# Kernel optimization log

Hardware: AMD Instinct MI355X
Metric: run time of the kernel (lower is better)

The kernel has to match this reference:

```python
import jax, jax.numpy as jnp
import numpy as np

D_MODEL = 1024
D_INNER = 1024
N_HEADS = 16
D_HEAD = D_INNER // N_HEADS
B = 2
CUR = 1024
PREV = 1024
LN_EPS = 1e-5


def _rel_shift(x):
    # x: (b, i, j, h) -- faithful to torch: pad along i, flat-reinterpret, drop first row
    b, i, j, h = x.shape
    zp = jnp.zeros((b, 1, j, h), x.dtype)
    xp = jnp.concatenate([zp, x], axis=1).reshape(i + 1, b, j, h)
    return xp[1:].reshape(b, i, j, h)


def setup_inputs() -> dict:
    key = jax.random.key(0)
    ks = jax.random.split(key, 10)
    x = jax.random.normal(ks[0], (B, CUR, D_MODEL), jnp.float32)
    mem = jax.random.normal(ks[1], (B, PREV, D_MODEL), jnp.float32)
    pos_emb = jax.random.normal(ks[2], (CUR + PREV, D_INNER), jnp.float32)
    u = jax.random.normal(ks[3], (N_HEADS, D_HEAD), jnp.float32) * 0.02
    v = jax.random.normal(ks[4], (N_HEADS, D_HEAD), jnp.float32) * 0.02
    # causal mask: query i (current segment) may attend key j if j <= i + PREV
    idx_i = jnp.arange(CUR)[:, None]
    idx_j = jnp.arange(CUR + PREV)[None, :]
    tgt_mask = jnp.broadcast_to((idx_j > idx_i + PREV)[None, :, :, None], (B, CUR, CUR + PREV, 1))
    Wq = jax.random.normal(ks[5], (D_INNER, D_MODEL), jnp.float32) * 0.02
    Wkv = jax.random.normal(ks[6], (2 * D_INNER, D_MODEL), jnp.float32) * 0.02
    Wfc = jax.random.normal(ks[7], (D_MODEL, D_INNER), jnp.float32) * 0.02
    bfc = jnp.zeros((D_MODEL,), jnp.float32)
    gamma = jnp.ones((D_MODEL,), jnp.float32)
    beta = jnp.zeros((D_MODEL,), jnp.float32)
    return {"x": x, "pos_emb": pos_emb, "u": u, "v": v, "mem": mem,
            "tgt_mask": tgt_mask, "Wq": Wq, "Wkv": Wkv, "Wfc": Wfc,
            "bfc": bfc, "gamma": gamma, "beta": beta}


def reference(x, pos_emb, u, v, mem, tgt_mask, Wq, Wkv, Wfc, bfc, gamma, beta):
    b, cur, _ = x.shape
    prev = mem.shape[1]
    tot = cur + prev
    h_telda = jnp.concatenate([mem, x], axis=1)               # (b, tot, d_model)
    q = jnp.einsum('bsm,im->bsi', x, Wq)                      # (b, cur, d_inner)
    kv = jnp.einsum('bsm,im->bsi', h_telda, Wkv)              # (b, tot, 2*d_inner)
    k, vv = kv[..., :D_INNER], kv[..., D_INNER:]
    q = q.reshape(b, cur, N_HEADS, D_HEAD)
    k = k.reshape(b, tot, N_HEADS, D_HEAD)
    vv = vv.reshape(b, tot, N_HEADS, D_HEAD)
    content = jnp.einsum('bihd,bjhd->bijh', q + u, k)
    pos = pos_emb.reshape(tot, N_HEADS, D_HEAD)
    pos_attn = jnp.einsum('bihd,jhd->bijh', q + v, pos)
    attn = content + _rel_shift(pos_attn)
    attn = jnp.where(tgt_mask, -jnp.inf, attn)
    attn = attn / (D_HEAD ** 0.5)
    attn = jax.nn.softmax(attn, axis=1)  # faithful: softmax over query dim as in original
    out = jnp.einsum('bijh,bjhd->bihd', attn, vv).reshape(b, cur, D_INNER)
    y = x + jnp.einsum('bsi,mi->bsm', out, Wfc) + bfc
    mu = jnp.mean(y, axis=-1, keepdims=True)
    var = jnp.mean((y - mu) ** 2, axis=-1, keepdims=True)
    return (y - mu) / jnp.sqrt(var + LN_EPS) * gamma + beta
```

## Files before the change

### kernel.cpp

```cpp
#include <hip/hip_runtime.h>
#include <hip/hip_bf16.h>
#include <stdint.h>

typedef unsigned short u16;
typedef __attribute__((ext_vector_type(8))) __bf16 bf16x8;
typedef __attribute__((ext_vector_type(4))) float f32x4;
typedef __attribute__((ext_vector_type(4))) float float4v;
typedef __attribute__((ext_vector_type(4))) u16  u16x4;

#define DEV __device__ __forceinline__

#define NB   2
#define CUR  1024
#define PREV 1024
#define TOT  2048
#define DM   1024
#define NH   16
#define DH   64

DEV u16 f2b(float f) {
    uint32_t u = __builtin_bit_cast(uint32_t, f);
    uint32_t r = (u + 0x7fffu + ((u >> 16) & 1u)) >> 16;
    return (u16)r;
}
DEV float b2f(u16 u) {
    return __builtin_bit_cast(float, (uint32_t)u << 16);
}

typedef const __attribute__((address_space(1))) void* gptr_t;
typedef __attribute__((address_space(3))) void*       lptr_t;
DEV void async16(const void* g, void* l) {
    __builtin_amdgcn_global_load_lds((gptr_t)g, (lptr_t)l, 16, 0, 0);
}

template<int BM, int BN, int BK, int WM, int WN, int EPI>
__global__ __launch_bounds__(256)
void gemm_bt(const u16* __restrict__ A, const u16* __restrict__ B,
             int M, int N, int K, long sA, long sB, int bzBase,
             void* __restrict__ C0, void* __restrict__ C1,
             const float* __restrict__ F0, const float* __restrict__ F1)
{
    constexpr int WAVES_N = BN / WN;
    constexpr int MI = WM / 16, NI = WN / 16;
    static_assert((BM / WM) * (BN / WN) == 4, "4 waves");
    static_assert(BK == 64, "swizzle assumes 8 chunks/row");

    __shared__ u16 lA[BM * BK];
    __shared__ u16 lB[BN * BK];

    const int bz = blockIdx.z;
    const int m0 = blockIdx.y * BM, n0 = blockIdx.x * BN;
    const int tid = threadIdx.x, wave = tid >> 6, lane = tid & 63;

    const u16* Ab = A + (long)bz * sA;
    const u16* Bb = B + (long)bz * sB;
    const int wm0 = (wave / WAVES_N) * WM, wn0 = (wave % WAVES_N) * WN;
    const int quad = lane >> 4;

    f32x4 acc[MI][NI];
#pragma unroll
    for (int mi = 0; mi < MI; ++mi)
#pragma unroll
        for (int ni = 0; ni < NI; ++ni)
            acc[mi][ni] = f32x4{0.f, 0.f, 0.f, 0.f};

    const int srow = tid >> 3;
    const int ksw  = (((tid & 7) ^ ((tid >> 3) & 7)) << 3);

    for (int kt = 0; kt < K; kt += BK) {
        __syncthreads();
#pragma unroll
        for (int is = 0; is < (BM * BK) / 2048; ++is) {
            int r = is * 32 + srow;
            async16(Ab + (long)(m0 + r) * K + kt + ksw, &lA[is * 2048 + wave * 512]);
        }
#pragma unroll
        for (int is = 0; is < (BN * BK) / 2048; ++is) {
            int r = is * 32 + srow;
            async16(Bb + (long)(n0 + r) * K + kt + ksw, &lB[is * 2048 + wave * 512]);
        }
        __syncthreads();
#pragma unroll
        for (int ks = 0; ks < BK; ks += 32) {
            bf16x8 af[MI], br[NI];
#pragma unroll
            for (int mi = 0; mi < MI; ++mi)
                af[mi] = *(const bf16x8*)(const void*)
                    &lA[(wm0 + mi * 16 + (lane & 15)) * BK +
                        ((((ks >> 3) + quad) ^ (lane & 7)) << 3)];
#pragma unroll
            for (int ni = 0; ni < NI; ++ni)
                br[ni] = *(const bf16x8*)(const void*)
                    &lB[(wn0 + ni * 16 + (lane & 15)) * BK +
                        ((((ks >> 3) + quad) ^ (lane & 7)) << 3)];
#pragma unroll
            for (int mi = 0; mi < MI; ++mi)
#pragma unroll
                for (int ni = 0; ni < NI; ++ni)
                    acc[mi][ni] = __builtin_amdgcn_mfma_f32_16x16x32_bf16(af[mi], br[ni], acc[mi][ni], 0, 0, 0);
        }
    }

    const int gbz = bzBase + bz;

    if constexpr (EPI == 1) {
        u16* Abuf = (u16*)C0;
        const int b = gbz;
#pragma unroll
        for (int mi = 0; mi < MI; ++mi) {
            const int m = m0 + wm0 + mi * 16 + quad * 4;
            const int h = m >> 6, d = m & 63;
            const float4v uu = *(const float4v*)(F0 + m);
            const float4v vv = *(const float4v*)(F1 + m);
#pragma unroll
            for (int ni = 0; ni < NI; ++ni) {
                const int i = n0 + wn0 + ni * 16 + (lane & 15);
                u16x4 pu, pv;
#pragma unroll
                for (int r = 0; r < 4; ++r) {
                    pu[r] = f2b(acc[mi][ni][r] + uu[r]);
                    pv[r] = f2b(acc[mi][ni][r] + vv[r]);
                }
                *(u16x4*)(Abuf + (((long)(b * NH + h)) * CUR + i) * 128 + d) = pu;
                if (b == 0) {
                    if (i > 0)
                        *(u16x4*)(Abuf + (((long)h) * CUR + (i - 1)) * 128 + 64 + d) = pv;
                    if (i == 1023) {
                        u16x4 z = {};
                        *(u16x4*)(Abuf + (((long)h) * CUR + 1023) * 128 + 64 + d) = z;
                    }
                } else {
                    *(u16x4*)(Abuf + (((long)(NH + h)) * CUR + i) * 128 + 64 + d) = pv;
                }
            }
        }
    } else if constexpr (EPI == 2) {
#pragma unroll
        for (int mi = 0; mi < MI; ++mi) {
            const int m = m0 + wm0 + mi * 16 + quad * 4;
            const bool isV = m >= DM;
            const int h = (m >> 6) & 15, d = m & 63;
#pragma unroll
            for (int ni = 0; ni < NI; ++ni) {
                const int n = n0 + wn0 + ni * 16 + (lane & 15);
                const int b = n >> 11, j = n & 2047;
                u16x4 p;
#pragma unroll
                for (int r = 0; r < 4; ++r) p[r] = f2b(acc[mi][ni][r]);
                if (!isV)
                    *(u16x4*)((u16*)C0 + (((long)(b * NH + h)) * TOT + j) * 128 + d) = p;
                else
                    *(u16x4*)((u16*)C1 + (((long)(b * NH + h)) * TOT + j) * 64 + d) = p;
            }
        }
    } else if constexpr (EPI == 5) {
#pragma unroll
        for (int mi = 0; mi < MI; ++mi) {
            const int m = m0 + wm0 + mi * 16 + quad * 4;
            const float4v bb = *(const float4v*)(F1 + m);
#pragma unroll
            for (int ni = 0; ni < NI; ++ni) {
                const int n = n0 + wn0 + ni * 16 + (lane & 15);
                const float4v xr = *(const float4v*)(F0 + (long)n * DM + m);
                float4v y;
#pragma unroll
                for (int r = 0; r < 4; ++r) y[r] = xr[r] + acc[mi][ni][r] + bb[r];
                *(float4v*)((float*)C0 + (long)n * DM + m) = y;
            }
        }
    }
}

template<int DO_PV>
__global__ __launch_bounds__(256)
void fused_attn(const u16* __restrict__ Abuf, const u16* __restrict__ Bbuf,
                const u16* __restrict__ Vp, const float* __restrict__ rcs,
                float* __restrict__ colsum, u16* __restrict__ Opart)
{
    __shared__ u16 lQ[64 * 128];
    __shared__ u16 lK[64 * 128];
    __shared__ u16 lV[DO_PV ? 64 * 64 : 1];
    __shared__ u16 lP[DO_PV ? 64 * 64 : 1];

    const int it = 15 - (int)blockIdx.x;
    const int bh = blockIdx.y;
    const int ch = blockIdx.z;
    const int n0 = it * 64;
    const int b = bh >> 4, h = bh & 15;
    const int tid = threadIdx.x, wave = tid >> 6, lane = tid & 63;
    const int l15 = lane & 15, quad = lane >> 4;
    const int iw = wave * 16 + l15;

    const u16*  Qg = Abuf + ((long)bh * CUR + n0) * 128;
    const u16*  Kg = Bbuf + (long)bh * TOT * 128;
    const u16*  Vg = Vp + (long)bh * DH * TOT;
    const float* rc = rcs + (long)bh * TOT;
    float* CS = colsum + (long)bh * TOT;

    const int r4 = tid >> 4, c4 = tid & 15;
    const int csQ = ((c4 & 8) | ((c4 & 7) ^ (r4 & 7)));
    const int r8 = tid >> 3;
    const int csV = (tid & 7) ^ (r8 & 7);

#pragma unroll
    for (int is = 0; is < 4; ++is)
        async16(Qg + (long)(is * 16 + r4) * 128 + csQ * 8, &lQ[is * 2048 + wave * 512]);

    f32x4 oacc[4];
#pragma unroll
    for (int mi = 0; mi < 4; ++mi) oacc[mi] = f32x4{0.f, 0.f, 0.f, 0.f};

    const int ig = n0 + iw;
    const int nt = it + 17;
    const int half = (nt + 1) >> 1;
    const int t0 = ch ? half : 0;
    const int t1 = ch ? nt : half;

    for (int t = t0; t < t1; ++t) {
        const int j0 = t * 64;
        __syncthreads();
        {
#pragma unroll
            for (int is = 0; is < 4; ++is)
                async16(Kg + (long)(j0 + is * 16 + r4) * 128 + csQ * 8,
                        &lK[is * 2048 + wave * 512]);
        }
        if constexpr (DO_PV) {
#pragma unroll
            for (int is = 0; is < 2; ++is)
                async16(Vg + (long)(is * 32 + r8) * TOT + j0 + csV * 8,
                        &lV[is * 2048 + wave * 512]);
        }
        __syncthreads();

        if constexpr (DO_PV) {
            f32x4 sacc[4];
#pragma unroll
            for (int smi = 0; smi < 4; ++smi) sacc[smi] = f32x4{0.f, 0.f, 0.f, 0.f};
#pragma unroll
            for (int ks = 0; ks < 128; ks += 32) {
                const int cq = (ks >> 3) + quad;
                const bf16x8 qf = *(const bf16x8*)(const void*)
                    &lQ[iw * 128 + (((cq & 8) | ((cq & 7) ^ (iw & 7))) << 3)];
#pragma unroll
                for (int smi = 0; smi < 4; ++smi) {
                    const int jr = smi * 16 + l15;
                    const bf16x8 kf = *(const bf16x8*)(const void*)
                        &lK[jr * 128 + (((cq & 8) | ((cq & 7) ^ (jr & 7))) << 3)];
                    sacc[smi] = __builtin_amdgcn_mfma_f32_16x16x32_bf16(kf, qf, sacc[smi], 0, 0, 0);
                }
            }
#pragma unroll
            for (int smi = 0; smi < 4; ++smi) {
                const int jl = smi * 16 + quad * 4;
                const int jg = j0 + jl;
                const float4v rcv = *(const float4v*)(rc + jg);
                u16x4 pk;
#pragma unroll
                for (int r = 0; r < 4; ++r) {
                    float p = (jg + r > ig + PREV) ? 0.f : __expf(sacc[smi][r] * 0.125f) * rcv[r];
                    pk[r] = f2b(p);
                }
                const int c16 = (jl >> 3) ^ (iw & 7);
                *(u16x4*)&lP[iw * 64 + (c16 << 3) + ((quad & 1) << 2)] = pk;
            }
#pragma unroll
            for (int ks = 0; ks < 64; ks += 32) {
                const int cp = (ks >> 3) + quad;
                const bf16x8 pb = *(const bf16x8*)(const void*)
                    &lP[iw * 64 + ((cp ^ (iw & 7)) << 3)];
#pragma unroll
                for (int mi = 0; mi < 4; ++mi) {
                    const int dr = mi * 16 + l15;
                    const bf16x8 vf = *(const bf16x8*)(const void*)
                        &lV[dr * 64 + ((cp ^ (dr & 7)) << 3)];
                    oacc[mi] = __builtin_amdgcn_mfma_f32_16x16x32_bf16(vf, pb, oacc[mi], 0, 0, 0);
                }
            }
        } else {
            f32x4 sacc[4];
#pragma unroll
            for (int smi = 0; smi < 4; ++smi) sacc[smi] = f32x4{0.f, 0.f, 0.f, 0.f};
#pragma unroll
            for (int ks = 0; ks < 128; ks += 32) {
                const int cq = (ks >> 3) + quad;
                const bf16x8 kf = *(const bf16x8*)(const void*)
                    &lK[iw * 128 + (((cq & 8) | ((cq & 7) ^ (iw & 7))) << 3)];
#pragma unroll
                for (int smi = 0; smi < 4; ++smi) {
                    const int ir = smi * 16 + l15;
                    const bf16x8 qf = *(const bf16x8*)(const void*)
                        &lQ[ir * 128 + (((cq & 8) | ((cq & 7) ^ (ir & 7))) << 3)];
                    sacc[smi] = __builtin_amdgcn_mfma_f32_16x16x32_bf16(qf, kf, sacc[smi], 0, 0, 0);
                }
            }
            const int jg = j0 + iw;
            float sum = 0.f;
#pragma unroll
            for (int smi = 0; smi < 4; ++smi) {
#pragma unroll
                for (int r = 0; r < 4; ++r) {
                    const int ii = n0 + smi * 16 + quad * 4 + r;
                    if (jg <= ii + PREV) sum += __expf(sacc[smi][r] * 0.125f);
                }
            }
            sum += __shfl_xor(sum, 16);
            sum += __shfl_xor(sum, 32);
            if (quad == 0) atomicAdd(CS + jg, sum);
        }
    }

    if constexpr (DO_PV) {
        u16* Ob = Opart + ((long)(ch * NB + b) * CUR) * DM + h * DH;
#pragma unroll
        for (int mi = 0; mi < 4; ++mi) {
            const int d = mi * 16 + quad * 4;
            u16x4 p;
#pragma unroll
            for (int r = 0; r < 4; ++r) p[r] = f2b(oacc[mi][r]);
            *(u16x4*)(Ob + (long)ig * DM + d) = p;
        }
    }
}

__global__ __launch_bounds__(256)
void combine_O(const u16* __restrict__ O0, const u16* __restrict__ O1,
               u16* __restrict__ Obf)
{
    int i = blockIdx.x * 256 + threadIdx.x;
    u16x4 a = ((const u16x4*)O0)[i];
    u16x4 c = ((const u16x4*)O1)[i];
    u16x4 o;
#pragma unroll
    for (int r = 0; r < 4; ++r) o[r] = f2b(b2f(a[r]) + b2f(c[r]));
    ((u16x4*)Obf)[i] = o;
}

__global__ __launch_bounds__(256)
void cvt_weights(const float* __restrict__ Wq, const float* __restrict__ Wkv,
                 const float* __restrict__ Wfc, u16* __restrict__ Wqb,
                 u16* __restrict__ Wkvb, u16* __restrict__ Wfcb)
{
    int i = blockIdx.x * 256 + threadIdx.x;
    const float* s; u16* d; int off;
    if (i < 262144)      { s = Wq;  d = Wqb;  off = i; }
    else if (i < 786432) { s = Wkv; d = Wkvb; off = i - 262144; }
    else                 { s = Wfc; d = Wfcb; off = i - 786432; }
    float4v f = ((const float4v*)s)[off];
    u16x4 o = {f2b(f[0]), f2b(f[1]), f2b(f[2]), f2b(f[3])};
    ((u16x4*)d)[off] = o;
}

__global__ __launch_bounds__(256)
void pack_H(const float* __restrict__ mem, const float* __restrict__ x, u16* __restrict__ dst)
{
    int i = blockIdx.x * 256 + threadIdx.x;
    int e = i << 2;
    int b = e >> 21, r = e & ((1 << 21) - 1);
    const float* src = (r < (1 << 20)) ? (mem + ((long)b << 20) + r)
                                       : (x + ((long)b << 20) + (r - (1 << 20)));
    float4v f = *(const float4v*)src;
    u16x4 o = {f2b(f[0]), f2b(f[1]), f2b(f[2]), f2b(f[3])};
    ((u16x4*)dst)[i] = o;
}

__global__ __launch_bounds__(256)
void pack_pos(const float* __restrict__ pos, u16* __restrict__ Bbuf)
{
    int i = blockIdx.x * 256 + threadIdx.x;
    int e = i << 2;
    int h = e >> 17, r = e & 131071, j = r >> 6, d = r & 63;
    float4v f = *(const float4v*)(pos + (long)j * DM + h * DH + d);
    u16x4 o = {f2b(f[0]), f2b(f[1]), f2b(f[2]), f2b(f[3])};
    long base = ((long)h * TOT + j) * 128 + 64 + d;
    *(u16x4*)(Bbuf + base) = o;
    *(u16x4*)(Bbuf + base + (long)NH * TOT * 128) = o;
}

__global__ __launch_bounds__(256)
void vprime_kernel(const u16* __restrict__ Vtmp, const float* __restrict__ colsum,
                   u16* __restrict__ Vp, float* __restrict__ rcs)
{
    __shared__ float t[64][65];
    int bz = blockIdx.y;
    int j0 = blockIdx.x * 64;
    const u16* src = Vtmp + ((long)bz * TOT + j0) * 64;
    const float* cs = colsum + (long)bz * TOT + j0;
    for (int e = threadIdx.x; e < 4096; e += 256) {
        int jl = e >> 6, d = e & 63;
        t[jl][d] = b2f(src[e]);
    }
    if (threadIdx.x < 64)
        rcs[(long)bz * TOT + j0 + threadIdx.x] = 1.f / cs[threadIdx.x];
    __syncthreads();
    u16* dst = Vp + (long)bz * DH * TOT + j0;
    for (int e = threadIdx.x; e < 4096; e += 256) {
        int d = e >> 6, jl = e & 63;
        dst[(long)d * TOT + jl] = f2b(t[jl][d]);
    }
}

__global__ __launch_bounds__(256)
void ln_kernel(const float* __restrict__ Y, const float* __restrict__ gamma,
               const float* __restrict__ beta, float* __restrict__ out)
{
    const int row = blockIdx.x;
    const float* y = Y + (long)row * DM;
    float v[4];
    float s = 0.f;
#pragma unroll
    for (int t = 0; t < 4; ++t) { v[t] = y[threadIdx.x + t * 256]; s += v[t]; }
#pragma unroll
    for (int off = 32; off > 0; off >>= 1) s += __shfl_down(s, off);
    __shared__ float r1[4], r2[4];
    int wv = threadIdx.x >> 6, ln = threadIdx.x & 63;
    if (ln == 0) r1[wv] = s;
    __syncthreads();
    float mu = (r1[0] + r1[1] + r1[2] + r1[3]) * (1.f / DM);
    float q = 0.f;
#pragma unroll
    for (int t = 0; t < 4; ++t) { float d = v[t] - mu; q += d * d; }
#pragma unroll
    for (int off = 32; off > 0; off >>= 1) q += __shfl_down(q, off);
    if (ln == 0) r2[wv] = q;
    __syncthreads();
    float var = (r2[0] + r2[1] + r2[2] + r2[3]) * (1.f / DM);
    float inv = rsqrtf(var + 1e-5f);
#pragma unroll
    for (int t = 0; t < 4; ++t) {
        int c = threadIdx.x + t * 256;
        out[(long)row * DM + c] = (v[t] - mu) * inv * gamma[c] + beta[c];
    }
}

extern "C" void kernel_launch(void* const* d_in, const int* in_sizes, int n_in,
                              void* d_out, int out_size, void* d_ws, size_t ws_size,
                              hipStream_t stream)
{
    const float* x     = (const float*)d_in[0];
    const float* pos   = (const float*)d_in[1];
    const float* u     = (const float*)d_in[2];
    const float* vbias = (const float*)d_in[3];
    const float* mem   = (const float*)d_in[4];
    const float* Wq    = (const float*)d_in[6];
    const float* Wkv   = (const float*)d_in[7];
    const float* Wfc   = (const float*)d_in[8];
    const float* bfc   = (const float*)d_in[9];
    const float* gamma = (const float*)d_in[10];
    const float* beta  = (const float*)d_in[11];
    float* out = (float*)d_out;

    char* w = (char*)d_ws;
    auto alloc = [&](size_t bytes) {
        char* p = w;
        w += (bytes + 255) & ~(size_t)255;
        return p;
    };
    u16*   Hb     = (u16*)alloc(4096UL * 1024 * 2);
    u16*   Wqb    = (u16*)alloc(1024UL * 1024 * 2);
    u16*   Wkvb   = (u16*)alloc(2048UL * 1024 * 2);
    u16*   Wfcb   = (u16*)alloc(1024UL * 1024 * 2);
    u16*   Abuf   = (u16*)alloc(32UL * 1024 * 128 * 2);
    u16*   Bbuf   = (u16*)alloc(32UL * 2048 * 128 * 2);
    u16*   Vtmp   = (u16*)alloc(32UL * 2048 * 64 * 2);
    u16*   Vp     = (u16*)alloc(32UL * 64 * 2048 * 2);
    float* colsum = (float*)alloc(32UL * 2048 * 4);
    float* rcs    = (float*)alloc(32UL * 2048 * 4);
    u16*   Opart  = (u16*)alloc(2UL * 2048 * 1024 * 2);
    u16*   Obf    = (u16*)alloc(2048UL * 1024 * 2);
    float* Yf     = (float*)alloc(2048UL * 1024 * 4);

    hipMemsetAsync(colsum, 0, 32UL * 2048 * 4, stream);

    cvt_weights<<<4096, 256, 0, stream>>>(Wq, Wkv, Wfc, Wqb, Wkvb, Wfcb);
    pack_H  <<<4096, 256, 0, stream>>>(mem, x, Hb);
    pack_pos<<<2048, 256, 0, stream>>>(pos, Bbuf);

    gemm_bt<128, 64, 64, 64, 32, 1><<<dim3(16, 8, 2), 256, 0, stream>>>(
        Wqb, Hb + 1024UL * 1024, 1024, 1024, 1024, 0, 2048L * 1024, 0,
        Abuf, nullptr, u, vbias);
    gemm_bt<128, 128, 64, 64, 64, 2><<<dim3(32, 16, 1), 256, 0, stream>>>(
        Wkvb, Hb, 2048, 4096, 1024, 0, 0, 0, Bbuf, Vtmp, nullptr, nullptr);

    fused_attn<0><<<dim3(16, 32, 2), 256, 0, stream>>>(
        Abuf, Bbuf, nullptr, nullptr, colsum, nullptr);
    vprime_kernel<<<dim3(32, 32), 256, 0, stream>>>(Vtmp, colsum, Vp, rcs);
    fused_attn<1><<<dim3(16, 32, 2), 256, 0, stream>>>(
        Abuf, Bbuf, Vp, rcs, nullptr, Opart);
    combine_O<<<2048, 256, 0, stream>>>(Opart, Opart + 2048UL * 1024, Obf);

    gemm_bt<64, 128, 64, 32, 64, 5><<<dim3(16, 16, 1), 256, 0, stream>>>(
        Wfcb, Obf, 1024, 2048, 1024, 0, 0, 0, Yf, nullptr, x, bfc);
    ln_kernel<<<2048, 256, 0, stream>>>(Yf, gamma, beta, out);
}
```

Baseline: 219.0 us.

## Restructure attention passes to keep K, P and V in registers

The two attention passes now split each 64-key tile across waves (16 keys per wave) instead of splitting query rows. K and V fragments are loaded straight from global memory into registers, and the softmax probabilities stay in registers as MFMA operands, so the per-tile LDS staging and block barriers go away. Each wave accumulates partial O for all 64 query rows, and the partials are summed across waves through LDS at the end. The reciprocal column-sum is now folded into V in vprime, which removes the rcs buffer. In exchange, the PV MFMAs run with half of their K-slots zero-padded, more global loads are uncoalesced, and the kernel holds a larger accumulator register footprint.

```diff
diff --git a/kernel.cpp b/kernel.cpp
--- a/kernel.cpp
+++ b/kernel.cpp
@@ -7,6 +7,7 @@
 typedef __attribute__((ext_vector_type(4))) float f32x4;
 typedef __attribute__((ext_vector_type(4))) float float4v;
 typedef __attribute__((ext_vector_type(4))) u16  u16x4;
+typedef __attribute__((ext_vector_type(8))) u16  u16x8;
 
 #define DEV __device__ __forceinline__
 
@@ -172,153 +173,153 @@
 }
 
 template<int DO_PV>
-__global__ __launch_bounds__(256)
-void fused_attn(const u16* __restrict__ Abuf, const u16* __restrict__ Bbuf,
-                const u16* __restrict__ Vp, const float* __restrict__ rcs,
-                float* __restrict__ colsum, u16* __restrict__ Opart)
+__global__ __launch_bounds__(256, 2)
+void attn2(const u16* __restrict__ Abuf, const u16* __restrict__ Bbuf,
+           const u16* __restrict__ Vp, float* __restrict__ colsum,
+           u16* __restrict__ Opart)
 {
     __shared__ u16 lQ[64 * 128];
-    __shared__ u16 lK[64 * 128];
-    __shared__ u16 lV[DO_PV ? 64 * 64 : 1];
-    __shared__ u16 lP[DO_PV ? 64 * 64 : 1];
+    __shared__ float lO[DO_PV ? 64 * 68 : 1];
 
     const int it = 15 - (int)blockIdx.x;
     const int bh = blockIdx.y;
     const int ch = blockIdx.z;
     const int n0 = it * 64;
-    const int b = bh >> 4, h = bh & 15;
     const int tid = threadIdx.x, wave = tid >> 6, lane = tid & 63;
     const int l15 = lane & 15, quad = lane >> 4;
-    const int iw = wave * 16 + l15;
-
-    const u16*  Qg = Abuf + ((long)bh * CUR + n0) * 128;
-    const u16*  Kg = Bbuf + (long)bh * TOT * 128;
-    const u16*  Vg = Vp + (long)bh * DH * TOT;
-    const float* rc = rcs + (long)bh * TOT;
+
+    const u16* Qg = Abuf + ((long)bh * CUR + n0) * 128;
+    const u16* Kg = Bbuf + (long)bh * TOT * 128;
+    const u16* Vg = Vp + (long)bh * DH * TOT;
     float* CS = colsum + (long)bh * TOT;
 
-    const int r4 = tid >> 4, c4 = tid & 15;
-    const int csQ = ((c4 & 8) | ((c4 & 7) ^ (r4 & 7)));
-    const int r8 = tid >> 3;
-    const int csV = (tid & 7) ^ (r8 & 7);
-
-#pragma unroll
-    for (int is = 0; is < 4; ++is)
-        async16(Qg + (long)(is * 16 + r4) * 128 + csQ * 8, &lQ[is * 2048 + wave * 512]);
-
-    f32x4 oacc[4];
-#pragma unroll
-    for (int mi = 0; mi < 4; ++mi) oacc[mi] = f32x4{0.f, 0.f, 0.f, 0.f};
-
-    const int ig = n0 + iw;
+    {
+        const int r4 = tid >> 4, c4 = tid & 15;
+        const int csQ = (c4 & 8) | ((c4 & 7) ^ (r4 & 7));
+#pragma unroll
+        for (int is = 0; is < 4; ++is)
+            async16(Qg + (long)(is * 16 + r4) * 128 + csQ * 8, &lQ[is * 2048 + wave * 512]);
+    }
+    __syncthreads();
+
+    f32x4 oacc[4][4];
+    if constexpr (DO_PV) {
+#pragma unroll
+        for (int mi = 0; mi < 4; ++mi)
+#pragma unroll
+            for (int smi = 0; smi < 4; ++smi)
+                oacc[mi][smi] = f32x4{0.f, 0.f, 0.f, 0.f};
+    }
+
+    const int jw = wave * 16;
     const int nt = it + 17;
     const int half = (nt + 1) >> 1;
     const int t0 = ch ? half : 0;
     const int t1 = ch ? nt : half;
 
     for (int t = t0; t < t1; ++t) {
-        const int j0 = t * 64;
-        __syncthreads();
-        {
-#pragma unroll
-            for (int is = 0; is < 4; ++is)
-                async16(Kg + (long)(j0 + is * 16 + r4) * 128 + csQ * 8,
-                        &lK[is * 2048 + wave * 512]);
-        }
+        const int jbase = t * 64 + jw;
+        const u16* Krow = Kg + (long)(jbase + l15) * 128 + quad * 8;
+        bf16x8 kreg[4];
+#pragma unroll
+        for (int c = 0; c < 4; ++c)
+            kreg[c] = *(const bf16x8*)(const void*)(Krow + c * 32);
+
+        f32x4 sacc[4];
+#pragma unroll
+        for (int smi = 0; smi < 4; ++smi) sacc[smi] = f32x4{0.f, 0.f, 0.f, 0.f};
+#pragma unroll
+        for (int c = 0; c < 4; ++c) {
+            const int cq = c * 4 + quad;
+#pragma unroll
+            for (int smi = 0; smi < 4; ++smi) {
+                const bf16x8 qf = *(const bf16x8*)(const void*)
+                    &lQ[(smi * 16 + l15) * 128 + (((cq & 8) | ((cq & 7) ^ (l15 & 7))) << 3)];
+                sacc[smi] = __builtin_amdgcn_mfma_f32_16x16x32_bf16(kreg[c], qf, sacc[smi], 0, 0, 0);
+            }
+        }
+
         if constexpr (DO_PV) {
-#pragma unroll
-            for (int is = 0; is < 2; ++is)
-                async16(Vg + (long)(is * 32 + r8) * TOT + j0 + csV * 8,
-                        &lV[is * 2048 + wave * 512]);
-        }
-        __syncthreads();
-
-        if constexpr (DO_PV) {
-            f32x4 sacc[4];
-#pragma unroll
-            for (int smi = 0; smi < 4; ++smi) sacc[smi] = f32x4{0.f, 0.f, 0.f, 0.f};
-#pragma unroll
-            for (int ks = 0; ks < 128; ks += 32) {
-                const int cq = (ks >> 3) + quad;
-                const bf16x8 qf = *(const bf16x8*)(const void*)
-                    &lQ[iw * 128 + (((cq & 8) | ((cq & 7) ^ (iw & 7))) << 3)];
-#pragma unroll
-                for (int smi = 0; smi < 4; ++smi) {
-                    const int jr = smi * 16 + l15;
-                    const bf16x8 kf = *(const bf16x8*)(const void*)
-                        &lK[jr * 128 + (((cq & 8) | ((cq & 7) ^ (jr & 7))) << 3)];
-                    sacc[smi] = __builtin_amdgcn_mfma_f32_16x16x32_bf16(kf, qf, sacc[smi], 0, 0, 0);
-                }
+            bf16x8 vf[4];
+#pragma unroll
+            for (int mi = 0; mi < 4; ++mi) {
+                const u16x4 vl = *(const u16x4*)(Vg + (long)(mi * 16 + l15) * TOT + jbase + quad * 4);
+                const u16x8 vraw = {vl[0], vl[1], vl[2], vl[3], 0, 0, 0, 0};
+                vf[mi] = __builtin_bit_cast(bf16x8, vraw);
             }
 #pragma unroll
             for (int smi = 0; smi < 4; ++smi) {
-                const int jl = smi * 16 + quad * 4;
-                const int jg = j0 + jl;
-                const float4v rcv = *(const float4v*)(rc + jg);
-                u16x4 pk;
-#pragma unroll
-                for (int r = 0; r < 4; ++r) {
-                    float p = (jg + r > ig + PREV) ? 0.f : __expf(sacc[smi][r] * 0.125f) * rcv[r];
-                    pk[r] = f2b(p);
-                }
-                const int c16 = (jl >> 3) ^ (iw & 7);
-                *(u16x4*)&lP[iw * 64 + (c16 << 3) + ((quad & 1) << 2)] = pk;
-            }
-#pragma unroll
-            for (int ks = 0; ks < 64; ks += 32) {
-                const int cp = (ks >> 3) + quad;
-                const bf16x8 pb = *(const bf16x8*)(const void*)
-                    &lP[iw * 64 + ((cp ^ (iw & 7)) << 3)];
-#pragma unroll
-                for (int mi = 0; mi < 4; ++mi) {
-                    const int dr = mi * 16 + l15;
-                    const bf16x8 vf = *(const bf16x8*)(const void*)
-                        &lV[dr * 64 + ((cp ^ (dr & 7)) << 3)];
-                    oacc[mi] = __builtin_amdgcn_mfma_f32_16x16x32_bf16(vf, pb, oacc[mi], 0, 0, 0);
-                }
+                const int ii = n0 + smi * 16 + l15;
+                u16 p0 = 0, p1 = 0, p2 = 0, p3 = 0;
+                const int jq = jbase + quad * 4;
+                if (jq + 0 <= ii + PREV) p0 = f2b(__expf(sacc[smi][0] * 0.125f));
+                if (jq + 1 <= ii + PREV) p1 = f2b(__expf(sacc[smi][1] * 0.125f));
+                if (jq + 2 <= ii + PREV) p2 = f2b(__expf(sacc[smi][2] * 0.125f));
+                if (jq + 3 <= ii + PREV) p3 = f2b(__expf(sacc[smi][3] * 0.125f));
+                const u16x8 praw = {p0, p1, p2, p3, 0, 0, 0, 0};
+                const bf16x8 pb = __builtin_bit_cast(bf16x8, praw);
+#pragma unroll
+                for (int mi = 0; mi < 4; ++mi)
+                    oacc[mi][smi] = __builtin_amdgcn_mfma_f32_16x16x32_bf16(vf[mi], pb, oacc[mi][smi], 0, 0, 0);
             }
         } else {
-            f32x4 sacc[4];
-#pragma unroll
-            for (int smi = 0; smi < 4; ++smi) sacc[smi] = f32x4{0.f, 0.f, 0.f, 0.f};
-#pragma unroll
-            for (int ks = 0; ks < 128; ks += 32) {
-                const int cq = (ks >> 3) + quad;
-                const bf16x8 kf = *(const bf16x8*)(const void*)
-                    &lK[iw * 128 + (((cq & 8) | ((cq & 7) ^ (iw & 7))) << 3)];
-#pragma unroll
-                for (int smi = 0; smi < 4; ++smi) {
-                    const int ir = smi * 16 + l15;
-                    const bf16x8 qf = *(const bf16x8*)(const void*)
-                        &lQ[ir * 128 + (((cq & 8) | ((cq & 7) ^ (ir & 7))) << 3)];
-                    sacc[smi] = __builtin_amdgcn_mfma_f32_16x16x32_bf16(qf, kf, sacc[smi], 0, 0, 0);
-                }
-            }
-            const int jg = j0 + iw;
-            float sum = 0.f;
+            float cs[4] = {0.f, 0.f, 0.f, 0.f};
+            const int jq = jbase + quad * 4;
 #pragma unroll
             for (int smi = 0; smi < 4; ++smi) {
-#pragma unroll
-                for (int r = 0; r < 4; ++r) {
-                    const int ii = n0 + smi * 16 + quad * 4 + r;
-                    if (jg <= ii + PREV) sum += __expf(sacc[smi][r] * 0.125f);
-                }
-            }
-            sum += __shfl_xor(sum, 16);
-            sum += __shfl_xor(sum, 32);
-            if (quad == 0) atomicAdd(CS + jg, sum);
+                const int ii = n0 + smi * 16 + l15;
+#pragma unroll
+                for (int r = 0; r < 4; ++r)
+                    if (jq + r <= ii + PREV) cs[r] += __expf(sacc[smi][r] * 0.125f);
+            }
+#pragma unroll
+            for (int r = 0; r < 4; ++r) {
+                cs[r] += __shfl_xor(cs[r], 1);
+                cs[r] += __shfl_xor(cs[r], 2);
+                cs[r] += __shfl_xor(cs[r], 4);
+                cs[r] += __shfl_xor(cs[r], 8);
+            }
+            if (l15 == 0) {
+                atomicAdd(CS + jq + 0, cs[0]);
+                atomicAdd(CS + jq + 1, cs[1]);
+                atomicAdd(CS + jq + 2, cs[2]);
+                atomicAdd(CS + jq + 3, cs[3]);
+            }
         }
     }
 
     if constexpr (DO_PV) {
+#pragma unroll
+        for (int wv = 0; wv < 4; ++wv) {
+            if (wave == wv) {
+#pragma unroll
+                for (int mi = 0; mi < 4; ++mi)
+#pragma unroll
+                    for (int smi = 0; smi < 4; ++smi) {
+                        const int i = smi * 16 + l15, d = mi * 16 + quad * 4;
+                        float* p = &lO[i * 68 + d];
+                        if (wv == 0) *(f32x4*)p = oacc[mi][smi];
+                        else {
+                            f32x4 cur = *(const f32x4*)p;
+#pragma unroll
+                            for (int r = 0; r < 4; ++r) cur[r] += oacc[mi][smi][r];
+                            *(f32x4*)p = cur;
+                        }
+                    }
+            }
+            __syncthreads();
+        }
+        const int b = bh >> 4, h = bh & 15;
         u16* Ob = Opart + ((long)(ch * NB + b) * CUR) * DM + h * DH;
 #pragma unroll
-        for (int mi = 0; mi < 4; ++mi) {
-            const int d = mi * 16 + quad * 4;
-            u16x4 p;
-#pragma unroll
-            for (int r = 0; r < 4; ++r) p[r] = f2b(oacc[mi][r]);
-            *(u16x4*)(Ob + (long)ig * DM + d) = p;
+        for (int k2 = 0; k2 < 4; ++k2) {
+            const int idx = k2 * 1024 + tid * 4;
+            const int il = idx >> 6, d = idx & 63;
+            const f32x4 vv = *(const f32x4*)&lO[il * 68 + d];
+            u16x4 o;
+#pragma unroll
+            for (int r = 0; r < 4; ++r) o[r] = f2b(vv[r]);
+            *(u16x4*)(Ob + (long)(n0 + il) * DM + d) = o;
         }
     }
 }
@@ -379,7 +380,7 @@
 
 __global__ __launch_bounds__(256)
 void vprime_kernel(const u16* __restrict__ Vtmp, const float* __restrict__ colsum,
-                   u16* __restrict__ Vp, float* __restrict__ rcs)
+                   u16* __restrict__ Vp)
 {
     __shared__ float t[64][65];
     int bz = blockIdx.y;
@@ -388,10 +389,8 @@
     const float* cs = colsum + (long)bz * TOT + j0;
     for (int e = threadIdx.x; e < 4096; e += 256) {
         int jl = e >> 6, d = e & 63;
-        t[jl][d] = b2f(src[e]);
-    }
-    if (threadIdx.x < 64)
-        rcs[(long)bz * TOT + j0 + threadIdx.x] = 1.f / cs[threadIdx.x];
+        t[jl][d] = b2f(src[e]) / cs[jl];
+    }
     __syncthreads();
     u16* dst = Vp + (long)bz * DH * TOT + j0;
     for (int e = threadIdx.x; e < 4096; e += 256) {
@@ -465,7 +464,6 @@
     u16*   Vtmp   = (u16*)alloc(32UL * 2048 * 64 * 2);
     u16*   Vp     = (u16*)alloc(32UL * 64 * 2048 * 2);
     float* colsum = (float*)alloc(32UL * 2048 * 4);
-    float* rcs    = (float*)alloc(32UL * 2048 * 4);
     u16*   Opart  = (u16*)alloc(2UL * 2048 * 1024 * 2);
     u16*   Obf    = (u16*)alloc(2048UL * 1024 * 2);
     float* Yf     = (float*)alloc(2048UL * 1024 * 4);
@@ -482,11 +480,11 @@
     gemm_bt<128, 128, 64, 64, 64, 2><<<dim3(32, 16, 1), 256, 0, stream>>>(
         Wkvb, Hb, 2048, 4096, 1024, 0, 0, 0, Bbuf, Vtmp, nullptr, nullptr);
 
-    fused_attn<0><<<dim3(16, 32, 2), 256, 0, stream>>>(
-        Abuf, Bbuf, nullptr, nullptr, colsum, nullptr);
-    vprime_kernel<<<dim3(32, 32), 256, 0, stream>>>(Vtmp, colsum, Vp, rcs);
-    fused_attn<1><<<dim3(16, 32, 2), 256, 0, stream>>>(
-        Abuf, Bbuf, Vp, rcs, nullptr, Opart);
+    attn2<0><<<dim3(16, 32, 2), 256, 0, stream>>>(
+        Abuf, Bbuf, nullptr, colsum, nullptr);
+    vprime_kernel<<<dim3(32, 32), 256, 0, stream>>>(Vtmp, colsum, Vp);
+    attn2<1><<<dim3(16, 32, 2), 256, 0, stream>>>(
+        Abuf, Bbuf, Vp, nullptr, Opart);
     combine_O<<<2048, 256, 0, stream>>>(Opart, Opart + 2048UL * 1024, Obf);
 
     gemm_bt<64, 128, 64, 32, 64, 5><<<dim3(16, 16, 1), 256, 0, stream>>>(
```

After: 201.4 us. -8.1%, faster.
